# Optimization experiments

Hardware: AMD Instinct MI355X
Metric: run time of the kernel (lower is better)

The kernel has to match this reference:

```python
import jax, jax.numpy as jnp
import numpy as np

B, T, F, U, S, M = 4, 64, 64, 64, 64, 64  # batch, timesteps, features, units, shape, memory_len


def setup_inputs() -> dict:
    key = jax.random.key(0)
    ks = jax.random.split(key, 8)
    return {
        "inputs":   jax.random.normal(ks[0], (B, T, F), jnp.float32),
        "Wk":       jax.random.normal(ks[1], (F, U), jnp.float32) / np.sqrt(F).astype(np.float32),
        "bk":       jax.random.normal(ks[2], (U,), jnp.float32) * 0.02,
        "Wv":       jax.random.normal(ks[3], (U, F), jnp.float32) / np.sqrt(U).astype(np.float32),
        "bv":       jax.random.normal(ks[4], (F,), jnp.float32) * 0.02,
        "w_s":      jax.random.normal(ks[5], (S,), jnp.float32),
        "mem_keys": jax.random.normal(ks[6], (M, T * F), jnp.float32) / np.sqrt(T * F).astype(np.float32),
        "mem_vals": jax.random.normal(ks[7], (M, F), jnp.float32),
    }


def hard_sigmoid(x):
    # keras hard_sigmoid: clip(0.2*x + 0.5, 0, 1)
    return jnp.clip(0.2 * x + 0.5, 0.0, 1.0)


def find_max_path(space):
    # space: [U, T, F, S] (per-sample; mirrors the tf.split-over-batch loop)
    score = space[:, :, :, -1].sum(axis=0)          # [T, F]  (K.sum over units axis)
    idx_f = jnp.argmax(score, axis=0)               # [F], values in [0, T)
    idx_t = jnp.argmax(score, axis=1)               # [T], values in [0, F)
    mp = jnp.take(space, idx_f, axis=-1)            # gather along S axis -> [U, T, F, F]
    mp = jnp.take(mp, idx_t, axis=0)                # gather along units axis -> [T, T, F, F]
    return mp.max(axis=0).max(axis=-1)              # [T, F]


def reference(inputs, Wk, bk, Wv, bv, w_s, mem_keys, mem_vals):
    # --- EventSpace: corrected context + rank-5 event space [B, U, T, F, S] ---
    h = jnp.tanh(inputs @ Wk + bk)                  # [B, T, U]
    output = h @ Wv + bv                            # [B, T, F] corrected context
    spaces = jnp.tanh(jnp.einsum('btu,btf,s->butfs', h, output, w_s))  # [B, U, T, F, S]

    # --- per-batch argmax + double gather retrieval ---
    max_spaces = jax.vmap(find_max_path)(spaces)    # [B, T, F]

    # --- QueueMemory: keys in T*F space, retrieve targets [B, F] + importance [B,1,1] ---
    flat = max_spaces.reshape(max_spaces.shape[0], -1)      # [B, T*F]
    attn = jax.nn.softmax(flat @ mem_keys.T, axis=-1)       # [B, M]
    targets = attn @ mem_vals                               # [B, F]
    importances = attn.max(axis=-1)[:, None, None]          # [B, 1, 1]

    # --- distance + tile ---
    dist = 0.5 - hard_sigmoid(
        jnp.linalg.norm(inputs - targets[:, None, :], axis=-1, keepdims=True))  # [B, T, 1]
    importances = jnp.tile(importances, (1, dist.shape[1], 1))                   # [B, T, 1]
    return dist, importances, output
```

## Files before the change

kernel.cpp:

```cpp
#include <hip/hip_runtime.h>
#include <math.h>

#define BB 4
#define T 64
#define F 64
#define U 64
#define S 64
#define M 64
#define UP 65
#define FP 65

#define WS_H    0
#define WS_SC   16384
#define WS_FLAT 32768
#define WS_LOG  49152

__device__ __forceinline__ float fast_tanh(float x) {
    float a = fabsf(x);
    float e = __builtin_amdgcn_exp2f(a * 2.88539008177792681f);
    float r = 1.0f - 2.0f * __builtin_amdgcn_rcpf(e + 1.0f);
    return copysignf(r, x);
}

__global__ __launch_bounds__(256) void kA_rows(
    const float* __restrict__ inputs, const float* __restrict__ Wk,
    const float* __restrict__ bk, const float* __restrict__ Wv,
    const float* __restrict__ bv, const float* __restrict__ w_s,
    float* __restrict__ ws, float* __restrict__ d_out)
{
    __shared__ float inp_s[F];
    __shared__ float part[4][64];
    __shared__ float h_s[U];
    __shared__ float out_s[F];

    const int blk = blockIdx.x;
    const int b = blk >> 6, t = blk & 63;
    const int tid = threadIdx.x;
    const int j = tid >> 6, l = tid & 63;
    const float w_last = w_s[S - 1];
    const float* inp = inputs + (b * T + t) * F;

    if (tid < F) inp_s[tid] = inp[tid];
    __syncthreads();

    {
        float acc = 0.0f;
        #pragma unroll
        for (int k = 0; k < 16; ++k) {
            int f = j * 16 + k;
            acc += inp_s[f] * Wk[f * U + l];
        }
        part[j][l] = acc;
    }
    __syncthreads();
    if (tid < U) {
        float v = part[0][tid] + part[1][tid] + part[2][tid] + part[3][tid] + bk[tid];
        float h = tanhf(v);
        h_s[tid] = h;
        ws[WS_H + (b * T + t) * U + tid] = h;
    }
    __syncthreads();

    {
        float acc = 0.0f;
        #pragma unroll
        for (int k = 0; k < 16; ++k) {
            int u = j * 16 + k;
            acc += h_s[u] * Wv[u * F + l];
        }
        part[j][l] = acc;
    }
    __syncthreads();
    if (tid < F) {
        float v = part[0][tid] + part[1][tid] + part[2][tid] + part[3][tid] + bv[tid];
        out_s[tid] = v;
        d_out[2 * BB * T + (b * T + t) * F + tid] = v;
    }
    __syncthreads();

    {
        float c = out_s[l] * w_last;
        float acc = 0.0f;
        #pragma unroll
        for (int k = 0; k < 16; ++k) {
            int u = j * 16 + k;
            acc += fast_tanh(h_s[u] * c);
        }
        part[j][l] = acc;
    }
    __syncthreads();
    if (tid < F) {
        ws[WS_SC + (b * T + t) * F + tid] =
            part[0][tid] + part[1][tid] + part[2][tid] + part[3][tid];
    }
}

__global__ __launch_bounds__(1024) void kB1_flat(
    const float* __restrict__ w_s, const float* __restrict__ ws_in,
    const float* __restrict__ d_out_const, float* __restrict__ ws)
{
    __shared__ float h_lds[T * UP];
    __shared__ float sc_lds[T * FP];
    __shared__ float out_lds[T * F];
    __shared__ int   idx_f[F];
    __shared__ int   idx_t[T];
    __shared__ float hmin_l[T], hmax_l[T];
    __shared__ float wext[2];

    const int b = blockIdx.x;
    const int tid = threadIdx.x;

    for (int e = 0; e < 4; ++e) {
        int id = e * 1024 + tid;
        int t = id >> 6, x = id & 63;
        sc_lds[t * FP + x] = ws_in[WS_SC + b * T * F + id];
        h_lds[t * UP + x]  = ws_in[WS_H + b * T * U + id];
        out_lds[id] = d_out_const[2 * BB * T + b * T * F + id];
    }
    __syncthreads();

    if (tid < F) {
        int f = tid;
        float best = sc_lds[f];
        int bi = 0;
        for (int t = 1; t < T; ++t) {
            float v = sc_lds[t * FP + f];
            if (v > best) { best = v; bi = t; }
        }
        idx_f[f] = bi;
    } else if (tid < 128) {
        int t = tid - 64;
        float best = sc_lds[t * FP];
        int bi = 0;
        for (int f = 1; f < F; ++f) {
            float v = sc_lds[t * FP + f];
            if (v > best) { best = v; bi = f; }
        }
        idx_t[t] = bi;
    }
    __syncthreads();

    if (tid < T) {
        int t = tid;
        float mn = 1e30f, mx = -1e30f;
        for (int i = 0; i < T; ++i) {
            float v = h_lds[t * UP + idx_t[i]];
            mn = fminf(mn, v);
            mx = fmaxf(mx, v);
        }
        hmin_l[t] = mn;
        hmax_l[t] = mx;
    } else if (tid == 64) {
        float mn = 1e30f, mx = -1e30f;
        for (int jj = 0; jj < F; ++jj) {
            float v = w_s[idx_f[jj]];
            mn = fminf(mn, v);
            mx = fmaxf(mx, v);
        }
        wext[0] = mn;
        wext[1] = mx;
    }
    __syncthreads();

    {
        float wmn = wext[0], wmx = wext[1];
        for (int e = 0; e < 4; ++e) {
            int id = e * 1024 + tid;
            int t = id >> 6;
            float q = out_lds[id];
            float hmn = hmin_l[t], hmx = hmax_l[t];
            float p1 = hmn * wmn, p2 = hmn * wmx, p3 = hmx * wmn, p4 = hmx * wmx;
            float pwmax = fmaxf(fmaxf(p1, p2), fmaxf(p3, p4));
            float pwmin = fminf(fminf(p1, p2), fminf(p3, p4));
            float mval = (q >= 0.0f) ? q * pwmax : q * pwmin;
            ws[WS_FLAT + b * T * F + id] = tanhf(mval);
        }
    }
}

__global__ __launch_bounds__(256) void kB2_logits(
    const float* __restrict__ mem_keys, const float* __restrict__ ws_in,
    float* __restrict__ ws)
{
    __shared__ float wsum[4];
    const int blk = blockIdx.x;
    const int b = blk >> 6, m = blk & 63;
    const int tid = threadIdx.x;
    const float* fl = ws_in + WS_FLAT + b * T * F;
    const float* mk = mem_keys + m * (T * F);

    float acc = 0.0f;
    #pragma unroll
    for (int i = 0; i < 16; ++i) {
        int k = i * 256 + tid;
        acc += fl[k] * mk[k];
    }
    #pragma unroll
    for (int off = 32; off; off >>= 1)
        acc += __shfl_down(acc, off, 64);
    if ((tid & 63) == 0) wsum[tid >> 6] = acc;
    __syncthreads();
    if (tid == 0)
        ws[WS_LOG + b * M + m] = wsum[0] + wsum[1] + wsum[2] + wsum[3];
}

__global__ __launch_bounds__(256) void kB3_head(
    const float* __restrict__ inputs, const float* __restrict__ mem_vals,
    const float* __restrict__ ws_in, float* __restrict__ d_out)
{
    __shared__ float attn[M];
    __shared__ float targets[F];
    __shared__ float imp_sh;

    const int b = blockIdx.x;
    const int tid = threadIdx.x;
    const float* inp = inputs + b * T * F;

    if (tid < M) {
        float l = ws_in[WS_LOG + b * M + tid];
        float mx = l;
        #pragma unroll
        for (int off = 32; off; off >>= 1)
            mx = fmaxf(mx, __shfl_xor(mx, off, 64));
        float e = __builtin_amdgcn_exp2f((l - mx) * 1.442695040888963f);
        float s = e;
        #pragma unroll
        for (int off = 32; off; off >>= 1)
            s += __shfl_xor(s, off, 64);
        attn[tid] = e / s;
        if (tid == 0) imp_sh = 1.0f / s;
    }
    __syncthreads();

    if (tid < F) {
        float acc = 0.0f;
        #pragma unroll 8
        for (int m = 0; m < M; ++m)
            acc += attn[m] * mem_vals[m * F + tid];
        targets[tid] = acc;
    }
    __syncthreads();

    {
        float imp = imp_sh;
        int t = tid >> 2;
        int j = tid & 3;
        float ss = 0.0f;
        #pragma unroll
        for (int k = 0; k < 16; ++k) {
            int f = j + 4 * k;
            float d = inp[t * F + f] - targets[f];
            ss += d * d;
        }
        ss += __shfl_down(ss, 2, 4);
        ss += __shfl_down(ss, 1, 4);
        if (j == 0) {
            float nrm = sqrtf(ss);
            float hs = fminf(0.2f * nrm + 0.5f, 1.0f);
            d_out[b * T + t] = 0.5f - hs;
            d_out[BB * T + b * T + t] = imp;
        }
    }
}

extern "C" void kernel_launch(void* const* d_in, const int* in_sizes, int n_in,
                              void* d_out, int out_size, void* d_ws, size_t ws_size,
                              hipStream_t stream) {
    const float* inputs   = (const float*)d_in[0];
    const float* Wk       = (const float*)d_in[1];
    const float* bk       = (const float*)d_in[2];
    const float* Wv       = (const float*)d_in[3];
    const float* bv       = (const float*)d_in[4];
    const float* w_s      = (const float*)d_in[5];
    const float* mem_keys = (const float*)d_in[6];
    const float* mem_vals = (const float*)d_in[7];
    float* out = (float*)d_out;
    float* ws  = (float*)d_ws;

    kA_rows<<<dim3(BB * T), dim3(256), 0, stream>>>(inputs, Wk, bk, Wv, bv, w_s, ws, out);
    kB1_flat<<<dim3(BB), dim3(1024), 0, stream>>>(w_s, ws, out, ws);
    kB2_logits<<<dim3(BB * M), dim3(256), 0, stream>>>(mem_keys, ws, ws);
    kB3_head<<<dim3(BB), dim3(256), 0, stream>>>(inputs, mem_vals, ws, out);
}
```

Baseline: 83.21 us.

## Fuse flat-space, memory logits, and softmax head into one per-batch kernel

Merges the three tail kernels (flat max-space, memory-key logits, softmax/targets/distance head) into a single 1024-thread block per batch. The flat T*F vector stays in LDS instead of round-tripping through workspace, and two launches are removed. In exchange, the 1 MB mem_keys dot products now run on only 4 blocks instead of 256, so that part of the work gets far less parallelism and bandwidth.

```diff
diff --git a/kernel.cpp b/kernel.cpp
--- a/kernel.cpp
+++ b/kernel.cpp
@@ -12,8 +12,6 @@
 
 #define WS_H    0
 #define WS_SC   16384
-#define WS_FLAT 32768
-#define WS_LOG  49152
 
 __device__ __forceinline__ float fast_tanh(float x) {
     float a = fabsf(x);
@@ -95,9 +93,10 @@
     }
 }
 
-__global__ __launch_bounds__(1024) void kB1_flat(
-    const float* __restrict__ w_s, const float* __restrict__ ws_in,
-    const float* __restrict__ d_out_const, float* __restrict__ ws)
+__global__ __launch_bounds__(1024) void kB_fused(
+    const float* __restrict__ inputs, const float* __restrict__ w_s,
+    const float* __restrict__ mem_keys, const float* __restrict__ mem_vals,
+    const float* __restrict__ ws_in, float* __restrict__ d_out)
 {
     __shared__ float h_lds[T * UP];
     __shared__ float sc_lds[T * FP];
@@ -106,16 +105,21 @@
     __shared__ int   idx_t[T];
     __shared__ float hmin_l[T], hmax_l[T];
     __shared__ float wext[2];
+    __shared__ float logits[M];
+    __shared__ float attn[M];
+    __shared__ float targets[F];
+    __shared__ float imp_sh;
 
     const int b = blockIdx.x;
     const int tid = threadIdx.x;
+    const float* inp = inputs + b * T * F;
 
     for (int e = 0; e < 4; ++e) {
         int id = e * 1024 + tid;
         int t = id >> 6, x = id & 63;
         sc_lds[t * FP + x] = ws_in[WS_SC + b * T * F + id];
         h_lds[t * UP + x]  = ws_in[WS_H + b * T * U + id];
-        out_lds[id] = d_out_const[2 * BB * T + b * T * F + id];
+        out_lds[id] = d_out[2 * BB * T + b * T * F + id];
     }
     __syncthreads();
 
@@ -173,56 +177,37 @@
             float pwmax = fmaxf(fmaxf(p1, p2), fmaxf(p3, p4));
             float pwmin = fminf(fminf(p1, p2), fminf(p3, p4));
             float mval = (q >= 0.0f) ? q * pwmax : q * pwmin;
-            ws[WS_FLAT + b * T * F + id] = tanhf(mval);
-        }
-    }
-}
-
-__global__ __launch_bounds__(256) void kB2_logits(
-    const float* __restrict__ mem_keys, const float* __restrict__ ws_in,
-    float* __restrict__ ws)
-{
-    __shared__ float wsum[4];
-    const int blk = blockIdx.x;
-    const int b = blk >> 6, m = blk & 63;
-    const int tid = threadIdx.x;
-    const float* fl = ws_in + WS_FLAT + b * T * F;
-    const float* mk = mem_keys + m * (T * F);
-
-    float acc = 0.0f;
-    #pragma unroll
-    for (int i = 0; i < 16; ++i) {
-        int k = i * 256 + tid;
-        acc += fl[k] * mk[k];
-    }
-    #pragma unroll
-    for (int off = 32; off; off >>= 1)
-        acc += __shfl_down(acc, off, 64);
-    if ((tid & 63) == 0) wsum[tid >> 6] = acc;
-    __syncthreads();
-    if (tid == 0)
-        ws[WS_LOG + b * M + m] = wsum[0] + wsum[1] + wsum[2] + wsum[3];
-}
-
-__global__ __launch_bounds__(256) void kB3_head(
-    const float* __restrict__ inputs, const float* __restrict__ mem_vals,
-    const float* __restrict__ ws_in, float* __restrict__ d_out)
-{
-    __shared__ float attn[M];
-    __shared__ float targets[F];
-    __shared__ float imp_sh;
-
-    const int b = blockIdx.x;
-    const int tid = threadIdx.x;
-    const float* inp = inputs + b * T * F;
-
-    if (tid < M) {
-        float l = ws_in[WS_LOG + b * M + tid];
-        float mx = l;
+            out_lds[id] = tanhf(mval);
+        }
+    }
+    __syncthreads();
+
+    {
+        int w = tid >> 6;
+        int l = tid & 63;
+        #pragma unroll
+        for (int mi = 0; mi < 4; ++mi) {
+            int m = w + 16 * mi;
+            const float* mk = mem_keys + m * (T * F);
+            float acc = 0.0f;
+            #pragma unroll 8
+            for (int i = 0; i < 64; ++i)
+                acc += out_lds[i * 64 + l] * mk[i * 64 + l];
+            #pragma unroll
+            for (int off = 32; off; off >>= 1)
+                acc += __shfl_down(acc, off, 64);
+            if (l == 0) logits[m] = acc;
+        }
+    }
+    __syncthreads();
+
+    if (tid < 64) {
+        float lg = logits[tid];
+        float mx = lg;
         #pragma unroll
         for (int off = 32; off; off >>= 1)
             mx = fmaxf(mx, __shfl_xor(mx, off, 64));
-        float e = __builtin_amdgcn_exp2f((l - mx) * 1.442695040888963f);
+        float e = __builtin_amdgcn_exp2f((lg - mx) * 1.442695040888963f);
         float s = e;
         #pragma unroll
         for (int off = 32; off; off >>= 1)
@@ -243,17 +228,18 @@
 
     {
         float imp = imp_sh;
-        int t = tid >> 2;
-        int j = tid & 3;
+        int t = tid >> 4;
+        int j = tid & 15;
         float ss = 0.0f;
         #pragma unroll
-        for (int k = 0; k < 16; ++k) {
-            int f = j + 4 * k;
+        for (int k = 0; k < 4; ++k) {
+            int f = j + 16 * k;
             float d = inp[t * F + f] - targets[f];
             ss += d * d;
         }
-        ss += __shfl_down(ss, 2, 4);
-        ss += __shfl_down(ss, 1, 4);
+        #pragma unroll
+        for (int off = 8; off; off >>= 1)
+            ss += __shfl_down(ss, off, 16);
         if (j == 0) {
             float nrm = sqrtf(ss);
             float hs = fminf(0.2f * nrm + 0.5f, 1.0f);
@@ -278,7 +264,5 @@
     float* ws  = (float*)d_ws;
 
     kA_rows<<<dim3(BB * T), dim3(256), 0, stream>>>(inputs, Wk, bk, Wv, bv, w_s, ws, out);
-    kB1_flat<<<dim3(BB), dim3(1024), 0, stream>>>(w_s, ws, out, ws);
-    kB2_logits<<<dim3(BB * M), dim3(256), 0, stream>>>(mem_keys, ws, ws);
-    kB3_head<<<dim3(BB), dim3(256), 0, stream>>>(inputs, mem_vals, ws, out);
-}
+    kB_fused<<<dim3(BB), dim3(1024), 0, stream>>>(inputs, w_s, mem_keys, mem_vals, ws, out);
+}
```

Measured after the change: 92.95 us. 11.7% more time.

## Fuse flat-space computation into memory-key logits kernel with per-block recompute

Applied to the files above, without the earlier changes.

Merges the per-batch max-path/flat kernel with the logits dot-product kernel. Each of the 256 blocks recomputes the argmax indices and flat values for its batch, then dots them directly with its prefetched mem_keys row held in registers. This removes one kernel launch and the workspace write/read of the flat tensor. In exchange, the argmax and extrema work is repeated 64 times per batch, and each block now needs large LDS.

```diff
diff --git a/kernel.cpp b/kernel.cpp
--- a/kernel.cpp
+++ b/kernel.cpp
@@ -12,8 +12,7 @@
 
 #define WS_H    0
 #define WS_SC   16384
-#define WS_FLAT 32768
-#define WS_LOG  49152
+#define WS_LOG  32768
 
 __device__ __forceinline__ float fast_tanh(float x) {
     float a = fabsf(x);
@@ -95,9 +94,10 @@
     }
 }
 
-__global__ __launch_bounds__(1024) void kB1_flat(
-    const float* __restrict__ w_s, const float* __restrict__ ws_in,
-    const float* __restrict__ d_out_const, float* __restrict__ ws)
+__global__ __launch_bounds__(256) void k2_flat_logits(
+    const float* __restrict__ w_s, const float* __restrict__ mem_keys,
+    const float* __restrict__ d_out_const, const float* __restrict__ ws_in,
+    float* __restrict__ ws)
 {
     __shared__ float h_lds[T * UP];
     __shared__ float sc_lds[T * FP];
@@ -106,12 +106,23 @@
     __shared__ int   idx_t[T];
     __shared__ float hmin_l[T], hmax_l[T];
     __shared__ float wext[2];
-
-    const int b = blockIdx.x;
+    __shared__ float wsum[4];
+
+    const int blk = blockIdx.x;
+    const int b = blk >> 6, m = blk & 63;
     const int tid = threadIdx.x;
 
-    for (int e = 0; e < 4; ++e) {
-        int id = e * 1024 + tid;
+    float mkr[16];
+    {
+        const float* mk = mem_keys + m * (T * F);
+        #pragma unroll
+        for (int i = 0; i < 16; ++i)
+            mkr[i] = mk[i * 256 + tid];
+    }
+
+    #pragma unroll
+    for (int i = 0; i < 16; ++i) {
+        int id = i * 256 + tid;
         int t = id >> 6, x = id & 63;
         sc_lds[t * FP + x] = ws_in[WS_SC + b * T * F + id];
         h_lds[t * UP + x]  = ws_in[WS_H + b * T * U + id];
@@ -162,10 +173,12 @@
     }
     __syncthreads();
 
+    float acc = 0.0f;
     {
         float wmn = wext[0], wmx = wext[1];
-        for (int e = 0; e < 4; ++e) {
-            int id = e * 1024 + tid;
+        #pragma unroll
+        for (int i = 0; i < 16; ++i) {
+            int id = i * 256 + tid;
             int t = id >> 6;
             float q = out_lds[id];
             float hmn = hmin_l[t], hmx = hmax_l[t];
@@ -173,27 +186,8 @@
             float pwmax = fmaxf(fmaxf(p1, p2), fmaxf(p3, p4));
             float pwmin = fminf(fminf(p1, p2), fminf(p3, p4));
             float mval = (q >= 0.0f) ? q * pwmax : q * pwmin;
-            ws[WS_FLAT + b * T * F + id] = tanhf(mval);
-        }
-    }
-}
-
-__global__ __launch_bounds__(256) void kB2_logits(
-    const float* __restrict__ mem_keys, const float* __restrict__ ws_in,
-    float* __restrict__ ws)
-{
-    __shared__ float wsum[4];
-    const int blk = blockIdx.x;
-    const int b = blk >> 6, m = blk & 63;
-    const int tid = threadIdx.x;
-    const float* fl = ws_in + WS_FLAT + b * T * F;
-    const float* mk = mem_keys + m * (T * F);
-
-    float acc = 0.0f;
-    #pragma unroll
-    for (int i = 0; i < 16; ++i) {
-        int k = i * 256 + tid;
-        acc += fl[k] * mk[k];
+            acc += tanhf(mval) * mkr[i];
+        }
     }
     #pragma unroll
     for (int off = 32; off; off >>= 1)
@@ -204,7 +198,7 @@
         ws[WS_LOG + b * M + m] = wsum[0] + wsum[1] + wsum[2] + wsum[3];
 }
 
-__global__ __launch_bounds__(256) void kB3_head(
+__global__ __launch_bounds__(256) void k3_head(
     const float* __restrict__ inputs, const float* __restrict__ mem_vals,
     const float* __restrict__ ws_in, float* __restrict__ d_out)
 {
@@ -278,7 +272,6 @@
     float* ws  = (float*)d_ws;
 
     kA_rows<<<dim3(BB * T), dim3(256), 0, stream>>>(inputs, Wk, bk, Wv, bv, w_s, ws, out);
-    kB1_flat<<<dim3(BB), dim3(1024), 0, stream>>>(w_s, ws, out, ws);
-    kB2_logits<<<dim3(BB * M), dim3(256), 0, stream>>>(mem_keys, ws, ws);
-    kB3_head<<<dim3(BB), dim3(256), 0, stream>>>(inputs, mem_vals, ws, out);
-}
+    k2_flat_logits<<<dim3(BB * M), dim3(256), 0, stream>>>(w_s, mem_keys, out, ws, ws);
+    k3_head<<<dim3(BB), dim3(256), 0, stream>>>(inputs, mem_vals, ws, out);
+}
```

After: 82.45 us (median of 2 runs). About the same (-0.9%).
